# Kernel optimization log

Hardware: AMD Instinct MI355X
Metric: run time of the kernel (lower is better)

Reference implementation:

```python
import jax, jax.numpy as jnp
import numpy as np

T, B, X, Y, H, Z, D = 256, 128, 128, 256, 512, 256, 8


def setup_inputs() -> dict:
    key = jax.random.key(0)
    ks = iter(jax.random.split(key, 64))

    def p(shape, scale=0.05):
        return jax.random.normal(next(ks), shape, dtype=jnp.float32) * scale

    inp = dict(
        x=p((T, B, X), 1.0), y=p((T, B, Y), 1.0),
        W_dprior=p((D, D)), b_dprior=p((D,)),
        Wdp=p((D, D, H)), bdp=p((D, D)),
        Wq1=p((D, Z, Z + H)), bq1=p((D, Z)), Wq2=p((D, Z, Z)), bq2=p((D, Z)),
        Wqm=p((D, Z, Z)), bqm=p((D, Z)), Wqs=p((D, Z, Z)), bqs=p((D, Z)),
        Wp1=p((D, Z, Z + H)), bp1=p((D, Z)), Wp2=p((D, Z, Z)), bp2=p((D, Z)),
        Wpm=p((D, Z, Z)), bpm=p((D, Z)), Wps=p((D, Z, Z)), bps=p((D, Z)),
        We1=p((D, Y, Z + H)), be1=p((D, Y)), We2=p((D, Y, Y)), be2=p((D, Y)),
        Wem=p((D, Y, Y)), bem=p((D, Y)), Wes=p((D, Y, Y)), bes=p((D, Y)),
        Wih_f=p((3 * H, X)), Whh_f=p((3 * H, H)), bih_f=p((3 * H,)), bhh_f=p((3 * H,)),
        Wih_b=p((3 * H, Y + H)), Whh_b=p((3 * H, H)), bih_b=p((3 * H,)), bhh_b=p((3 * H,)),
    )
    return inp


def _gru(xs, Wih, Whh, bih, bhh):
    # xs: [T, B, in]; torch GRU gate order r, z, n
    h0 = jnp.zeros((xs.shape[1], Whh.shape[1]), xs.dtype)

    def cell(h, x_t):
        gi = x_t @ Wih.T + bih
        gh = h @ Whh.T + bhh
        ir, iz, inn = jnp.split(gi, 3, axis=1)
        hr, hz, hn = jnp.split(gh, 3, axis=1)
        r = jax.nn.sigmoid(ir + hr)
        zg = jax.nn.sigmoid(iz + hz)
        n = jnp.tanh(inn + r * hn)
        h_new = (1.0 - zg) * n + zg * h
        return h_new, h_new

    _, out = jax.lax.scan(cell, h0, xs)
    return out  # [T, B, H]


def _mlp2(W1, b1, W2, b2, inp):
    # inp: [B, in]; W1: [D, out, in] -> [D, B, out] with two ReLU layers
    h = jax.nn.relu(jnp.einsum('doi,bi->dbo', W1, inp) + b1[:, None, :])
    return jax.nn.relu(jnp.einsum('doi,dbi->dbo', W2, h) + b2[:, None, :])


def _head(Wm, bm, h):
    return jnp.einsum('doi,dbi->dbo', Wm, h) + bm[:, None, :]


def reference(x, y, W_dprior, b_dprior, Wdp, bdp,
              Wq1, bq1, Wq2, bq2, Wqm, bqm, Wqs, bqs,
              Wp1, bp1, Wp2, bp2, Wpm, bpm, Wps, bps,
              We1, be1, We2, be2, Wem, bem, Wes, bes,
              Wih_f, Whh_f, bih_f, bhh_f, Wih_b, Whh_b, bih_b, bhh_b):
    Tn, Bn, _ = x.shape
    Dn = W_dprior.shape[0]
    Zn = Wq1.shape[1]
    eye = jnp.eye(Dn, dtype=x.dtype)
    T0 = eye * (1.0 - 0.05 * Dn) + 0.05  # Transition_initial
    Trans = jax.nn.softmax(T0 @ W_dprior.T + b_dprior, axis=1) * 0.5 + eye * 0.5
    logT = jnp.log(Trans)

    of = _gru(x, Wih_f, Whh_f, bih_f, bhh_f)                       # [T,B,H]
    ob = _gru(jnp.flip(jnp.concatenate([y, of], 2), 0), Wih_b, Whh_b, bih_b, bhh_b)
    ob = jnp.flip(ob, 0)  # ob[t] == output_backward[T-1-t]

    d0 = jax.nn.one_hot(jax.random.categorical(jax.random.key(7), jnp.zeros((Bn, Dn))), Dn, dtype=x.dtype)
    z0 = jnp.zeros((Bn, Zn), x.dtype)
    dpost0 = jnp.full((Bn, Dn), 1.0 / Dn, x.dtype)

    def step(carry, inputs):
        d_prev, z_prev, dpost_prev, key = carry
        of_t, ob_t, y_t = inputs
        key, k1, k2 = jax.random.split(key, 3)

        # per-expert d-posterior, mixed by previous one-hot state
        dpost_all = jax.nn.softmax(jnp.einsum('dij,bj->dbi', Wdp, ob_t) + bdp[:, None, :], axis=-1)  # [D,B,D]
        d_post = jnp.einsum('dbi,bd->bi', dpost_all, d_prev)  # [B,D]
        d_new = jax.nn.one_hot(jax.random.categorical(k1, jnp.log(d_post)), Dn, dtype=x.dtype)

        # z prior (transition) experts
        hp = _mlp2(Wp1, bp1, Wp2, bp2, jnp.concatenate([of_t, z_prev], 1))
        zp_mean = _head(Wpm, bpm, hp)
        zp_std = jax.nn.softplus(_head(Wps, bps, hp))
        # z posterior experts
        hq = _mlp2(Wq1, bq1, Wq2, bq2, jnp.concatenate([ob_t, z_prev], 1))
        zq_mean = _head(Wqm, bqm, hq)
        zq_std = jax.nn.softplus(_head(Wqs, bqs, hq))

        zq_mean_mix = jnp.einsum('dbz,bd->bz', zq_mean, d_new)
        zq_std_mix = jnp.einsum('dbz,bd->bz', zq_std, d_new)
        z_t = zq_mean_mix + zq_std_mix * jax.random.normal(k2, zq_mean_mix.shape, x.dtype)

        # emission experts
        he = _mlp2(We1, be1, We2, be2, jnp.concatenate([of_t, z_t], 1))
        ye_mean = _head(Wem, bem, he)
        ye_std = jax.nn.softplus(_head(Wes, bes, he))

        # losses, weighted per expert as in the torch loop
        kldg_e = 2.0 * jnp.log(zp_std / zq_std) + (zq_std ** 2 + (zq_mean - zp_mean) ** 2) / zp_std ** 2 - 1.0
        kldg = 0.5 * jnp.einsum('dbz,bd->', kldg_e, d_post)
        kldc_e = jnp.sum(dpost_all * (jnp.log(dpost_all + 1e-8) - logT[:, None, :]), axis=-1)  # [D,B]
        kldc = jnp.einsum('db,bd->', kldc_e, dpost_prev)
        nll_e = 0.5 * (jnp.log(2.0 * jnp.pi) + 2.0 * jnp.log(ye_std) + ((y_t - ye_mean) / ye_std) ** 2)
        nll = jnp.einsum('dby,bd->', nll_e, d_post)

        return (d_new, z_t, d_post, key), (kldg, kldc, nll)

    carry0 = (d0, z0, dpost0, jax.random.key(1))
    _, (kg, kc, nl) = jax.lax.scan(step, carry0, (of, ob, y))
    return jnp.stack([jnp.sum(kg), jnp.sum(kc), jnp.sum(nl)])
```

## Files before the change

### kernel.cpp

```cpp
#include <hip/hip_runtime.h>
#include <hip/hip_bf16.h>
#include <math.h>
#include <stdint.h>

#define TT 256
#define BB 128
#define XX 128
#define YY 256
#define HH 512
#define ZZ 256
#define DD 8
#define G3 1536
#define CH 8
#define TC 32

typedef unsigned int u32;
typedef __attribute__((ext_vector_type(8))) short bf16x8;
typedef __attribute__((ext_vector_type(4))) float f32x4;

__device__ __forceinline__ uint2 tf2(uint2 key, u32 c0, u32 c1) {
  u32 ks0 = key.x, ks1 = key.y, ks2 = ks0 ^ ks1 ^ 0x1BD11BDAu;
  u32 x0 = c0 + ks0, x1 = c1 + ks1;
#define TFR(r) { x0 += x1; x1 = (x1 << r) | (x1 >> (32 - r)); x1 ^= x0; }
  TFR(13) TFR(15) TFR(26) TFR(6)  x0 += ks1; x1 += ks2 + 1u;
// ... 68 lines not shown
__device__ __forceinline__ float b2f(u32 h) { return __uint_as_float(h << 16); }

__device__ __forceinline__ short f2b(float f) {
  __hip_bfloat16 h = __float2bfloat16(f);
  return *reinterpret_cast<short*>(&h);
}

#define FMA8M(v0, v1, wv, A) do { \
  A[0]=fmaf((v0).x,(wv),A[0]); A[1]=fmaf((v0).y,(wv),A[1]); \
  A[2]=fmaf((v0).z,(wv),A[2]); A[3]=fmaf((v0).w,(wv),A[3]); \
  A[4]=fmaf((v1).x,(wv),A[4]); A[5]=fmaf((v1).y,(wv),A[5]); \
  A[6]=fmaf((v1).z,(wv),A[6]); A[7]=fmaf((v1).w,(wv),A[7]); } while(0)

#define FMA44(a4, b4, A) do { \
  A[0][0]=fmaf((a4).x,(b4).x,A[0][0]); A[0][1]=fmaf((a4).x,(b4).y,A[0][1]); A[0][2]=fmaf((a4).x,(b4).z,A[0][2]); A[0][3]=fmaf((a4).x,(b4).w,A[0][3]); \
  A[1][0]=fmaf((a4).y,(b4).x,A[1][0]); A[1][1]=fmaf((a4).y,(b4).y,A[1][1]); A[1][2]=fmaf((a4).y,(b4).z,A[1][2]); A[1][3]=fmaf((a4).y,(b4).w,A[1][3]); \
  A[2][0]=fmaf((a4).z,(b4).x,A[2][0]); A[2][1]=fmaf((a4).z,(b4).y,A[2][1]); A[2][2]=fmaf((a4).z,(b4).z,A[2][2]); A[2][3]=fmaf((a4).z,(b4).w,A[2][3]); \
  A[3][0]=fmaf((a4).w,(b4).x,A[3][0]); A[3][1]=fmaf((a4).w,(b4).y,A[3][1]); A[3][2]=fmaf((a4).w,(b4).z,A[3][2]); A[3][3]=fmaf((a4).w,(b4).w,A[3][3]); } while(0)

__global__ void k_sentinel(float* __restrict__ out) {
  if (threadIdx.x < 3) out[threadIdx.x] = 1.2345e8f;
}

__global__ void k_init1(const float* __restrict__ Wdpr, const float* __restrict__ bdpr,
                        float* __restrict__ LOGT, uint2* __restrict__ KEYS,
                        uint2* __restrict__ K1s, uint2* __restrict__ K2s) {
  int tid = threadIdx.x;
  if (tid == 0) {
    uint2 key; key.x = 0u; key.y = 1u;
    for (int t = 0; t < TT; t++) {
      KEYS[t] = key;
      uint2 e0 = tf2(key, 0u, 3u);
      uint2 e1 = tf2(key, 1u, 4u);
      key.x = e0.x; key.y = e1.x;
    }
  }
  __syncthreads();
  for (int t = tid; t < TT; t += 256) {
    uint2 key = KEYS[t];
    uint2 e0 = tf2(key, 0u, 3u);
    uint2 e1 = tf2(key, 1u, 4u);
    uint2 e2 = tf2(key, 2u, 5u);
    uint2 k1; k1.x = e2.x; k1.y = e0.y;
    uint2 k2; k2.x = e1.y; k2.y = e2.y;
    K1s[t] = k1; K2s[t] = k2;
  }
// ... 11 lines not shown
    LOGT[i * 8 + j] = logf(tr);
  }
}

__global__ void k_init2(int* __restrict__ EIDX, float* __restrict__ DP, float* __restrict__ ZT) {
  int blk = blockIdx.x, tid = threadIdx.x;
  if (blk == 0) {
    if (tid < BB) {
      uint2 k7; k7.x = 0u; k7.y = 7u;
      float best = -1e30f; int bi = 0;
      for (int i = 0; i < DD; i++) {
        float g = gumbelf(rbits(k7, tid * DD + i, BB * DD));
        if (g > best) { best = g; bi = i; }
      }
      EIDX[tid] = bi;
      for (int i = 0; i < DD; i++) DP[tid * DD + i] = 0.125f;
    }
  } else {
    int base = (blk - 1) * 1024 + tid;
    ZT[base] = 0.f; ZT[base + 256] = 0.f; ZT[base + 512] = 0.f; ZT[base + 768] = 0.f;
  }
}

template <int ACT, int OUTBF, int A0BF>
__global__ __launch_bounds__(256)
void gemm2seg(const void* __restrict__ A0v, long a0_gs, int lda0, int K0,
              const float* __restrict__ A1, long a1_gs, int lda1, int K1,
              const float* __restrict__ W, long w_gs, int ldw, int wofs,
              const float* __restrict__ bias, long b_gs,
              void* __restrict__ Cv, long c_gs, int ldc, int gdiv) {
  const int g = blockIdx.z;
  const int ga = g / gdiv, gw = g % DD;
  const float* pW = W + (long)gw * w_gs + wofs;
  const int m0 = blockIdx.x * 64, n0 = blockIdx.y * 64;
  const int tid = threadIdx.x;
  const int tm = tid >> 4, tn = tid & 15;
  __shared__ float As[32][68];
  __shared__ float Bs[32][68];
  float acc[4][4];
#pragma unroll
  for (int r = 0; r < 4; r++)
#pragma unroll
    for (int c = 0; c < 4; c++) acc[r][c] = 0.f;
  const int K = K0 + K1;
  for (int kb = 0; kb < K; kb += 32) {
#pragma unroll
    for (int l = 0; l < 2; l++) {
      int idx = tid + l * 256; int row = idx >> 3, c4 = (idx & 7) << 2;
      float4 v;
      if (kb < K0) {
        if (A0BF) {
          const __hip_bfloat16* p = (const __hip_bfloat16*)A0v + (long)ga * a0_gs + (long)(m0 + row) * lda0 + kb + c4;
          uint2 u = *(const uint2*)p;
          v.x = b2f(u.x & 0xffffu); v.y = b2f(u.x >> 16);
          v.z = b2f(u.y & 0xffffu); v.w = b2f(u.y >> 16);
        } else {
          v = *(const float4*)((const float*)A0v + (long)ga * a0_gs + (long)(m0 + row) * lda0 + kb + c4);
        }
      } else {
        v = *(const float4*)(A1 + (long)ga * a1_gs + (long)(m0 + row) * lda1 + (kb - K0) + c4);
      }
      As[c4 + 0][row] = v.x; As[c4 + 1][row] = v.y; As[c4 + 2][row] = v.z; As[c4 + 3][row] = v.w;
    }
#pragma unroll
    for (int l = 0; l < 2; l++) {
      int idx = tid + l * 256; int row = idx >> 3, c4 = (idx & 7) << 2;
      float4 v = *(const float4*)(pW + (long)(n0 + row) * ldw + kb + c4);
      Bs[c4 + 0][row] = v.x; Bs[c4 + 1][row] = v.y; Bs[c4 + 2][row] = v.z; Bs[c4 + 3][row] = v.w;
    }
    __syncthreads();
#pragma unroll
    for (int k = 0; k < 32; k++) {
      float4 a = *(const float4*)&As[k][tm << 2];
      float4 b = *(const float4*)&Bs[k][tn << 2];
      FMA44(a, b, acc);
    }
    __syncthreads();
  }
#pragma unroll
  for (int r = 0; r < 4; r++) {
    int m = m0 + (tm << 2) + r;
#pragma unroll
    for (int c = 0; c < 4; c++) {
      int n = n0 + (tn << 2) + c;
      float v = acc[r][c];
      if (bias) v += bias[(long)gw * b_gs + n];
      if (ACT == 1) v = fmaxf(v, 0.f);
      if (OUTBF) ((__hip_bfloat16*)Cv)[(long)g * c_gs + (long)m * ldc + n] = __float2bfloat16(v);
      else       ((float*)Cv)[(long)g * c_gs + (long)m * ldc + n] = v;
    }
  }
}

template <int ACT, int OUTBF, int A0BF>
__global__ __launch_bounds__(256)
void gemmMF(const void* __restrict__ A0v, long a0_gs, int lda0, int K0,
            const float* __restrict__ A1, long a1_gs, int lda1, int K1,
            const float* __restrict__ W, long w_gs, int ldw, int wofs,
            const float* __restrict__ bias, long b_gs,
            void* __restrict__ Cv, long c_gs, int ldc, int gdiv) {
  const int g = blockIdx.z;
  const int ga = g / gdiv, gw = g % DD;
  const float* pW = W + (long)gw * w_gs + wofs;
  const int m0 = blockIdx.x * 64, n0 = blockIdx.y * 64;
  const int tid = threadIdx.x;
  const int wave = tid >> 6, lane = tid & 63;
  const int wr = wave >> 1, wc = wave & 1;
  __shared__ short As[64][40];
  __shared__ short Bs[64][40];
  f32x4 acc[2][2];
#pragma unroll
  for (int a = 0; a < 2; a++)
#pragma unroll
    for (int b = 0; b < 2; b++) acc[a][b] = (f32x4)(0.f);
  const int K = K0 + K1;
  const int srow = tid >> 2;
  const int sks  = (tid & 3) << 3;
  for (int kb = 0; kb < K; kb += 32) {
    {
      bf16x8 st;
      if (kb < K0) {
        if (A0BF) {
          const short* p = (const short*)A0v + (long)ga * a0_gs + (long)(m0 + srow) * lda0 + kb + sks;
          st = *(const bf16x8*)p;
        } else {
          const float* p = (const float*)A0v + (long)ga * a0_gs + (long)(m0 + srow) * lda0 + kb + sks;
          float4 v0 = *(const float4*)p, v1 = *(const float4*)(p + 4);
          st[0]=f2b(v0.x); st[1]=f2b(v0.y); st[2]=f2b(v0.z); st[3]=f2b(v0.w);
          st[4]=f2b(v1.x); st[5]=f2b(v1.y); st[6]=f2b(v1.z); st[7]=f2b(v1.w);
        }
      } else {
        const float* p = A1 + (long)ga * a1_gs + (long)(m0 + srow) * lda1 + (kb - K0) + sks;
        float4 v0 = *(const float4*)p, v1 = *(const float4*)(p + 4);
        st[0]=f2b(v0.x); st[1]=f2b(v0.y); st[2]=f2b(v0.z); st[3]=f2b(v0.w);
        st[4]=f2b(v1.x); st[5]=f2b(v1.y); st[6]=f2b(v1.z); st[7]=f2b(v1.w);
      }
      *(bf16x8*)&As[srow][sks] = st;
    }
    {
      const float* p = pW + (long)(n0 + srow) * ldw + kb + sks;
      float4 v0 = *(const float4*)p, v1 = *(const float4*)(p + 4);
      bf16x8 st;
      st[0]=f2b(v0.x); st[1]=f2b(v0.y); st[2]=f2b(v0.z); st[3]=f2b(v0.w);
      st[4]=f2b(v1.x); st[5]=f2b(v1.y); st[6]=f2b(v1.z); st[7]=f2b(v1.w);
      *(bf16x8*)&Bs[srow][sks] = st;
    }
    __syncthreads();
    {
      const int l15 = lane & 15, kq = (lane >> 4) << 3;
      bf16x8 a0 = *(const bf16x8*)&As[wr * 32 + l15][kq];
      bf16x8 a1 = *(const bf16x8*)&As[wr * 32 + 16 + l15][kq];
      bf16x8 b0 = *(const bf16x8*)&Bs[wc * 32 + l15][kq];
      bf16x8 b1 = *(const bf16x8*)&Bs[wc * 32 + 16 + l15][kq];
      acc[0][0] = __builtin_amdgcn_mfma_f32_16x16x32_bf16(a0, b0, acc[0][0], 0, 0, 0);
      acc[0][1] = __builtin_amdgcn_mfma_f32_16x16x32_bf16(a0, b1, acc[0][1], 0, 0, 0);
      acc[1][0] = __builtin_amdgcn_mfma_f32_16x16x32_bf16(a1, b0, acc[1][0], 0, 0, 0);
      acc[1][1] = __builtin_amdgcn_mfma_f32_16x16x32_bf16(a1, b1, acc[1][1], 0, 0, 0);
    }
    __syncthreads();
  }
  const int ccol = lane & 15, crow4 = (lane >> 4) << 2;
#pragma unroll
  for (int mr = 0; mr < 2; mr++) {
#pragma unroll
    for (int nc = 0; nc < 2; nc++) {
      int n = n0 + wc * 32 + nc * 16 + ccol;
      float bv = bias ? bias[(long)gw * b_gs + n] : 0.f;
#pragma unroll
      for (int r = 0; r < 4; r++) {
        int m = m0 + wr * 32 + mr * 16 + crow4 + r;
        float v = acc[mr][nc][r] + bv;
        if (ACT == 1) v = fmaxf(v, 0.f);
        if (OUTBF) ((__hip_bfloat16*)Cv)[(long)g * c_gs + (long)m * ldc + n] = __float2bfloat16(v);
        else       ((float*)Cv)[(long)g * c_gs + (long)m * ldc + n] = v;
      }
    }
  }
}

__global__ __launch_bounds__(256)
void k_gru(const float* __restrict__ GI, const float* __restrict__ hprev,
           const float* __restrict__ Whh, const float* __restrict__ bhh,
           float* __restrict__ hout, __hip_bfloat16* __restrict__ houtB) {
  const int bt = blockIdx.x >> 5, jt = blockIdx.x & 31;
  const int b0 = bt * 16, j0 = jt * 16;
  const int tid = threadIdx.x;
  const int bi = tid >> 4, ji = tid & 15;
  __shared__ float ws[48][132];
  __shared__ float hs[16][132];
  float ar = 0.f, az = 0.f, an = 0.f;
  for (int kc = 0; kc < HH; kc += 128) {
    for (int idx = tid; idx < 48 * 32; idx += 256) {
      int r = idx >> 5, c4 = (idx & 31) << 2;
      int jr = r / 3, gr = r % 3;
      int grow = gr * HH + j0 + jr;
      *(float4*)&ws[r][c4] = *(const float4*)(Whh + (long)grow * HH + kc + c4);
    }
    for (int idx = tid; idx < 16 * 32; idx += 256) {
      int r = idx >> 5, c4 = (idx & 31) << 2;
// ... 167 lines not shown
#pragma unroll
    for (int bl = 0; bl < 8; bl++) { qm[bl] = bm_; qs[bl] = bs__; }
    for (int k = 0; k < ZZ; k += 4) {
      float4 wm4 = *(const float4*)(wm + k);
      float4 ws4 = *(const float4*)(wsd + k);
#pragma unroll
      for (int kk = 0; kk < 4; kk++) {
        float wmv = kk == 0 ? wm4.x : kk == 1 ? wm4.y : kk == 2 ? wm4.z : wm4.w;
        float wsv = kk == 0 ? ws4.x : kk == 1 ? ws4.y : kk == 2 ? ws4.z : ws4.w;
        float4 h0 = *(const float4*)&h2t[k + kk][0];
        float4 h1v = *(const float4*)&h2t[k + kk][4];
        FMA8M(h0, h1v, wmv, qm);
        FMA8M(h0, h1v, wsv, qs);
      }
    }
  }
#pragma unroll
  for (int bl = 0; bl < 8; bl++) {
    if (en_s[bl] == d) {
      int b = b0 + bl;
      float eps = normalf(rbits(K2s[t], b * ZZ + tid, BB * ZZ));
      ZT[((long)(t + 1) * BB + b) * ZZ + tid] = qm[bl] + softplusf_(qs[bl]) * eps;
    }
  }
}

__global__ __launch_bounds__(256)
void k_heads_pq(const float* __restrict__ LA, const float* __restrict__ LB,
                const float* __restrict__ Wpm, const float* __restrict__ bpm,
                const float* __restrict__ Wps, const float* __restrict__ bps,
                const float* __restrict__ Wqm, const float* __restrict__ bqm,
                const float* __restrict__ Wqs, const float* __restrict__ bqs,
                const float* __restrict__ DP, float* __restrict__ PART, int t0) {
  const int g = blockIdx.z; const int tl = g >> 3, d = g & 7; const int t = t0 + tl;
  const int m0 = blockIdx.x * 64, n0 = blockIdx.y * 64;
  const int tid = threadIdx.x; const int tm = tid >> 4, tn = tid & 15;
  __shared__ float As[32][68], W1s[32][68], W2s[32][68];
  float aPm[4][4], aPs[4][4], aQm[4][4], aQs[4][4];
#pragma unroll
  for (int r = 0; r < 4; r++)
#pragma unroll
    for (int c = 0; c < 4; c++) { aPm[r][c] = 0.f; aPs[r][c] = 0.f; aQm[r][c] = 0.f; aQs[r][c] = 0.f; }

#define HEADPASS(Abase, Wm_, Ws_, ACCM, ACCS) \
  { const float* Ap = (Abase) + (long)g * (BB * ZZ); \
    const float* Wm = (Wm_) + (long)d * ZZ * ZZ; \
    const float* Wsp = (Ws_) + (long)d * ZZ * ZZ; \
    for (int kb = 0; kb < ZZ; kb += 32) { \
      for (int l = 0; l < 2; l++) { \
        int idx = tid + l * 256; int row = idx >> 3, c4 = (idx & 7) << 2; \
        float4 v = *(const float4*)(Ap + (long)(m0 + row) * ZZ + kb + c4); \
        As[c4+0][row]=v.x; As[c4+1][row]=v.y; As[c4+2][row]=v.z; As[c4+3][row]=v.w; \
        v = *(const float4*)(Wm + (long)(n0 + row) * ZZ + kb + c4); \
        W1s[c4+0][row]=v.x; W1s[c4+1][row]=v.y; W1s[c4+2][row]=v.z; W1s[c4+3][row]=v.w; \
        v = *(const float4*)(Wsp + (long)(n0 + row) * ZZ + kb + c4); \
        W2s[c4+0][row]=v.x; W2s[c4+1][row]=v.y; W2s[c4+2][row]=v.z; W2s[c4+3][row]=v.w; \
      } \
      __syncthreads(); \
      _Pragma("unroll") \
      for (int k = 0; k < 32; k++) { \
        float4 a = *(const float4*)&As[k][tm << 2]; \
        float4 b1 = *(const float4*)&W1s[k][tn << 2]; \
        float4 b2 = *(const float4*)&W2s[k][tn << 2]; \
        FMA44(a, b1, ACCM); \
        FMA44(a, b2, ACCS); \
      } \
      __syncthreads(); \
    } }

  HEADPASS(LA, Wpm, Wps, aPm, aPs)
  HEADPASS(LB, Wqm, Wqs, aQm, aQs)

  float local = 0.f;
#pragma unroll
  for (int r = 0; r < 4; r++) {
    int b = m0 + (tm << 2) + r;
    float w8 = DP[((long)(t + 1) * BB + b) * DD + d];
#pragma unroll
    for (int c = 0; c < 4; c++) {
      int n = n0 + (tn << 2) + c;
      float pm = aPm[r][c] + bpm[d * ZZ + n];
      float ps = softplusf_(aPs[r][c] + bps[d * ZZ + n]);
      float qm = aQm[r][c] + bqm[d * ZZ + n];
      float qs = softplusf_(aQs[r][c] + bqs[d * ZZ + n]);
      float dm = qm - pm;
      local += 0.5f * w8 * (2.f * logf(ps / qs) + (qs * qs + dm * dm) / (ps * ps) - 1.f);
    }
  }
  local = wave_sum(local);
  __shared__ float red[4];
  int wid = tid >> 6;
  if ((tid & 63) == 0) red[wid] = local;
  __syncthreads();
  if (tid == 0) atomicAdd(&PART[((long)t * DD + d) * 4 + 0], red[0] + red[1] + red[2] + red[3]);
}

__global__ __launch_bounds__(256)
void k_heads_e(const float* __restrict__ LA,
               const float* __restrict__ Wem, const float* __restrict__ bem,
               const float* __restrict__ Wes, const float* __restrict__ bes,
               const float* __restrict__ yy, const float* __restrict__ DP,
               const float* __restrict__ KCE, float* __restrict__ PART, int t0) {
  const int g = blockIdx.z; const int tl = g >> 3, d = g & 7; const int t = t0 + tl;
  const int m0 = blockIdx.x * 64, n0 = blockIdx.y * 64;
  const int tid = threadIdx.x; const int tm = tid >> 4, tn = tid & 15;
  __shared__ float As[32][68], W1s[32][68], W2s[32][68];
  float aM[4][4], aS[4][4];
#pragma unroll
  for (int r = 0; r < 4; r++)
#pragma unroll
    for (int c = 0; c < 4; c++) { aM[r][c] = 0.f; aS[r][c] = 0.f; }
  {
    const float* Ap = LA + (long)g * (BB * ZZ);
    const float* Wm = Wem + (long)d * YY * YY;
    const float* Wsp = Wes + (long)d * YY * YY;
    for (int kb = 0; kb < YY; kb += 32) {
      for (int l = 0; l < 2; l++) {
        int idx = tid + l * 256; int row = idx >> 3, c4 = (idx & 7) << 2;
        float4 v = *(const float4*)(Ap + (long)(m0 + row) * YY + kb + c4);
        As[c4+0][row]=v.x; As[c4+1][row]=v.y; As[c4+2][row]=v.z; As[c4+3][row]=v.w;
        v = *(const float4*)(Wm + (long)(n0 + row) * YY + kb + c4);
        W1s[c4+0][row]=v.x; W1s[c4+1][row]=v.y; W1s[c4+2][row]=v.z; W1s[c4+3][row]=v.w;
        v = *(const float4*)(Wsp + (long)(n0 + row) * YY + kb + c4);
        W2s[c4+0][row]=v.x; W2s[c4+1][row]=v.y; W2s[c4+2][row]=v.z; W2s[c4+3][row]=v.w;
      }
      __syncthreads();
#pragma unroll
      for (int k = 0; k < 32; k++) {
        float4 a = *(const float4*)&As[k][tm << 2];
        float4 b1 = *(const float4*)&W1s[k][tn << 2];
        float4 b2 = *(const float4*)&W2s[k][tn << 2];
        FMA44(a, b1, aM);
        FMA44(a, b2, aS);
      }
      __syncthreads();
    }
  }
  float local = 0.f;
#pragma unroll
  for (int r = 0; r < 4; r++) {
    int b = m0 + (tm << 2) + r;
    float w8 = DP[((long)(t + 1) * BB + b) * DD + d];
#pragma unroll
    for (int c = 0; c < 4; c++) {
      int n = n0 + (tn << 2) + c;
      float ym = aM[r][c] + bem[d * YY + n];
      float ys = softplusf_(aS[r][c] + bes[d * YY + n]);
      float yv = yy[((long)t * BB + b) * YY + n];
      float rr = (yv - ym) / ys;
      local += w8 * 0.5f * (1.8378770664093453f + 2.f * logf(ys) + rr * rr);
    }
  }
  local = wave_sum(local);
  __shared__ float red[4];
  int wid = tid >> 6;
  if ((tid & 63) == 0) red[wid] = local;
  __syncthreads();
  if (tid == 0) atomicAdd(&PART[((long)t * DD + d) * 4 + 2], red[0] + red[1] + red[2] + red[3]);
  if (blockIdx.x == 0 && blockIdx.y == 0) {
    __syncthreads();
    float v = 0.f;
    if (tid < BB) v = KCE[((long)t * DD + d) * BB + tid] * DP[((long)t * BB + tid) * DD + d];
    v = wave_sum(v);
    if ((tid & 63) == 0) red[wid] = v;
    __syncthreads();
    if (tid == 0) atomicAdd(&PART[((long)t * DD + d) * 4 + 1], red[0] + red[1] + red[2] + red[3]);
  }
}

__global__ void k_fin(const float* __restrict__ PART, float* __restrict__ out) {
  int tid = threadIdx.x;
  float s0 = 0.f, s1 = 0.f, s2 = 0.f;
  for (int i = tid; i < TT * DD; i += 256) {
    s0 += PART[i * 4 + 0]; s1 += PART[i * 4 + 1]; s2 += PART[i * 4 + 2];
  }
  s0 = wave_sum(s0); s1 = wave_sum(s1); s2 = wave_sum(s2);
  __shared__ float r0[4], r1[4], r2[4];
  int wid = tid >> 6;
  if ((tid & 63) == 0) { r0[wid] = s0; r1[wid] = s1; r2[wid] = s2; }
  __syncthreads();
  if (tid == 0) {
    out[0] = r0[0] + r0[1] + r0[2] + r0[3];
    out[1] = r1[0] + r1[1] + r1[2] + r1[3];
    out[2] = r2[0] + r2[1] + r2[2] + r2[3];
  }
}

extern "C" void kernel_launch(void* const* d_in, const int* in_sizes, int n_in,
                              void* d_out, int out_size, void* d_ws, size_t ws_size,
// ... 39 lines not shown
  const float* bhh_b  = (const float*)d_in[37];

  char* base = (char*)d_ws;
  size_t off = 0;
  auto alloc = [&](size_t bytes) -> char* {
    char* p = base + off;
    off += (bytes + 1023) & ~(size_t)1023;
    return p;
  };
  float* LOGT = (float*)alloc(64 * 4);
  uint2* KEYS = (uint2*)alloc(TT * 8);
  uint2* K1s  = (uint2*)alloc(TT * 8);
  uint2* K2s  = (uint2*)alloc(TT * 8);
  int*   EIDX = (int*)alloc((size_t)(TT + 1) * BB * 4);
  float* DP   = (float*)alloc((size_t)(TT + 1) * BB * DD * 4);
  float* DPA  = (float*)alloc((size_t)TT * BB * DD * DD * 4);
  float* KCE  = (float*)alloc((size_t)TT * DD * BB * 4);
  float* ZT   = (float*)alloc((size_t)(TT + 1) * BB * ZZ * 4);
  float* PART = (float*)alloc((size_t)TT * DD * 4 * 4);
  float* OF   = (float*)alloc((size_t)TT * BB * HH * 4);
  __hip_bfloat16* OB = (__hip_bfloat16*)alloc((size_t)TT * BB * HH * 2);
  float* HROLL = (float*)alloc((size_t)TC * BB * HH * 4);
  char*  SH   = alloc((size_t)TC * BB * G3 * 4);
  float* GIc  = (float*)SH;
  __hip_bfloat16* OBPc = (__hip_bfloat16*)SH;
  float* LH1  = (float*)SH;
  float* LH2A = LH1 + (size_t)CH * DD * BB * ZZ;
  float* LH2B = LH2A + (size_t)CH * DD * BB * ZZ;

  if (ws_size < off) {
    k_sentinel<<<1, 64, 0, stream>>>((float*)d_out);
    return;
  }

  hipMemsetAsync(PART, 0, (size_t)TT * DD * 4 * 4, stream);
  k_init1<<<1, 256, 0, stream>>>(Wdpr, bdpr, LOGT, KEYS, K1s, K2s);
  k_init2<<<33, 256, 0, stream>>>(EIDX, DP, ZT);

  const long BH = (long)BB * HH, BZ = (long)BB * ZZ, BG = (long)BB * G3;

  for (int c = 0; c < TT / TC; c++) {
    int t0 = c * TC;
    gemm2seg<0, 0, 0><<<dim3(64, 24, 1), 256, 0, stream>>>(
        x + (long)t0 * BB * XX, 0, XX, XX, nullptr, 0, 4, 0,
        Wih_f, 0, XX, 0, bih_f, 0, GIc, 0, G3, 1);
    for (int tl = 0; tl < TC; tl++) {
      int t = t0 + tl;
      k_gru<<<256, 256, 0, stream>>>(GIc + (long)tl * BG,
                                     t ? (OF + (long)(t - 1) * BH) : nullptr,
                                     Whh_f, bhh_f, OF + (long)t * BH, nullptr);
    }
  }
  for (int c = TT / TC - 1; c >= 0; c--) {
    int t0 = c * TC;
    gemm2seg<0, 0, 0><<<dim3(64, 24, 1), 256, 0, stream>>>(
        y + (long)t0 * BB * YY, 0, YY, YY, OF + (long)t0 * BH, 0, HH, HH,
        Wih_b, 0, 768, 0, bih_b, 0, GIc, 0, G3, 1);
    for (int tl = TC - 1; tl >= 0; tl--) {
      int t = t0 + tl;
      k_gru<<<256, 256, 0, stream>>>(GIc + (long)tl * BG,
                                     (t == TT - 1) ? nullptr : (HROLL + (long)((t + 1) & (TC - 1)) * BH),
                                     Whh_b, bhh_b, HROLL + (long)(t & (TC - 1)) * BH, OB + (long)t * BH);
    }
    k_dpa<<<dim3(TC, 4), 256, 0, stream>>>(Wdp, bdp, HROLL, LOGT, DPA, KCE, t0);
  }
  k_dchain<<<1, 128, 0, stream>>>(DPA, K1s, EIDX, DP);
  for (int c = 0; c < TT / TC; c++) {
    int t0 = c * TC;
    gemmMF<0, 1, 1><<<dim3(64, 4, 8), 256, 0, stream>>>(
        OB + (long)t0 * BH, 0, HH, HH, nullptr, 0, 4, 0,
        Wq1, (long)ZZ * 768, 768, 0, nullptr, 0, OBPc, (long)TC * BB * ZZ, ZZ, 8);
    for (int tl = 0; tl < TC; tl++) {
      k_step<<<128, 256, 0, stream>>>(t0 + tl, EIDX, K2s, OBPc,
                                      Wq1, bq1, Wq2, bq2, Wqm, bqm, Wqs, bqs, ZT);
    }
  }
  for (int c = 0; c < TT / CH; c++) {
    int t0 = c * CH;
    dim3 gl(2, 4, CH * DD);
    gemmMF<1, 0, 0><<<gl, 256, 0, stream>>>(
        OF + (long)t0 * BH, BH, HH, HH, ZT + (long)t0 * BZ, BZ, ZZ, ZZ,
        Wp1, (long)ZZ * 768, 768, 0, bp1, ZZ, LH1, BZ, ZZ, 8);
    gemmMF<1, 0, 0><<<gl, 256, 0, stream>>>(
        LH1, BZ, ZZ, ZZ, nullptr, 0, 4, 0,
        Wp2, (long)ZZ * ZZ, ZZ, 0, bp2, ZZ, LH2A, BZ, ZZ, 1);
    gemmMF<1, 0, 1><<<gl, 256, 0, stream>>>(
        OB + (long)t0 * BH, BH, HH, HH, ZT + (long)t0 * BZ, BZ, ZZ, ZZ,
        Wq1, (long)ZZ * 768, 768, 0, bq1, ZZ, LH1, BZ, ZZ, 8);
    gemmMF<1, 0, 0><<<gl, 256, 0, stream>>>(
        LH1, BZ, ZZ, ZZ, nullptr, 0, 4, 0,
        Wq2, (long)ZZ * ZZ, ZZ, 0, bq2, ZZ, LH2B, BZ, ZZ, 1);
    k_heads_pq<<<gl, 256, 0, stream>>>(LH2A, LH2B, Wpm, bpm, Wps, bps,
                                       Wqm, bqm, Wqs, bqs, DP, PART, t0);
    gemmMF<1, 0, 0><<<gl, 256, 0, stream>>>(
        OF + (long)t0 * BH, BH, HH, HH, ZT + (long)(t0 + 1) * BZ, BZ, ZZ, ZZ,
        We1, (long)YY * 768, 768, 0, be1, YY, LH1, BZ, ZZ, 8);
    gemmMF<1, 0, 0><<<gl, 256, 0, stream>>>(
        LH1, BZ, ZZ, ZZ, nullptr, 0, 4, 0,
        We2, (long)YY * YY, YY, 0, be2, YY, LH2A, BZ, ZZ, 1);
    k_heads_e<<<gl, 256, 0, stream>>>(LH2A, Wem, bem, Wes, bes, y, DP, KCE, PART, t0);
  }
  k_fin<<<1, 256, 0, stream>>>(PART, (float*)d_out);
}
```

Baseline: 27.06 ms.

## Pre-convert expert weights to bf16 and move loss heads onto MFMA

Adds a conversion kernel that casts all expert MLP and head weights to bf16 once per call. The gemmMF kernels then load bf16 weights directly instead of converting on every tile. Intermediate activations are stored as bf16, and the fp32 FMA-based p/q and emission head kernels are replaced with MFMA bf16 versions. This cuts global bandwidth and conversion ALU work in the per-chunk expert loop, at the cost of lower precision in the intermediates and heads.

```diff
diff --git a/kernel.cpp b/kernel.cpp
--- a/kernel.cpp
+++ b/kernel.cpp
@@ -114,6 +114,16 @@
   if (threadIdx.x < 3) out[threadIdx.x] = 1.2345e8f;
 }
 
+__global__ void k_cvt(const float* __restrict__ s, __hip_bfloat16* __restrict__ d, int n4) {
+  int i = blockIdx.x * 256 + threadIdx.x;
+  int stride = gridDim.x * 256;
+  for (; i < n4; i += stride) {
+    const float4 v = *(const float4*)(s + (size_t)i * 4);
+    short4 o; o.x = f2b(v.x); o.y = f2b(v.y); o.z = f2b(v.z); o.w = f2b(v.w);
+    *(short4*)((short*)d + (size_t)i * 4) = o;
+  }
+}
+
 __global__ void k_init1(const float* __restrict__ Wdpr, const float* __restrict__ bdpr,
                         float* __restrict__ LOGT, uint2* __restrict__ KEYS,
                         uint2* __restrict__ K1s, uint2* __restrict__ K2s) {
@@ -171,9 +181,9 @@
   }
 }
 
-template <int ACT, int OUTBF, int A0BF>
+template <int ACT, int OUTBF>
 __global__ __launch_bounds__(256)
-void gemm2seg(const void* __restrict__ A0v, long a0_gs, int lda0, int K0,
+void gemm2seg(const float* __restrict__ A0, long a0_gs, int lda0, int K0,
               const float* __restrict__ A1, long a1_gs, int lda1, int K1,
               const float* __restrict__ W, long w_gs, int ldw, int wofs,
               const float* __restrict__ bias, long b_gs,
@@ -198,14 +208,7 @@
       int idx = tid + l * 256; int row = idx >> 3, c4 = (idx & 7) << 2;
       float4 v;
       if (kb < K0) {
-        if (A0BF) {
-          const __hip_bfloat16* p = (const __hip_bfloat16*)A0v + (long)ga * a0_gs + (long)(m0 + row) * lda0 + kb + c4;
-          uint2 u = *(const uint2*)p;
-          v.x = b2f(u.x & 0xffffu); v.y = b2f(u.x >> 16);
-          v.z = b2f(u.y & 0xffffu); v.w = b2f(u.y >> 16);
-        } else {
-          v = *(const float4*)((const float*)A0v + (long)ga * a0_gs + (long)(m0 + row) * lda0 + kb + c4);
-        }
+        v = *(const float4*)(A0 + (long)ga * a0_gs + (long)(m0 + row) * lda0 + kb + c4);
       } else {
         v = *(const float4*)(A1 + (long)ga * a1_gs + (long)(m0 + row) * lda1 + (kb - K0) + c4);
       }
@@ -245,12 +248,12 @@
 __global__ __launch_bounds__(256)
 void gemmMF(const void* __restrict__ A0v, long a0_gs, int lda0, int K0,
             const float* __restrict__ A1, long a1_gs, int lda1, int K1,
-            const float* __restrict__ W, long w_gs, int ldw, int wofs,
+            const __hip_bfloat16* __restrict__ W, long w_gs, int ldw, int wofs,
             const float* __restrict__ bias, long b_gs,
             void* __restrict__ Cv, long c_gs, int ldc, int gdiv) {
   const int g = blockIdx.z;
   const int ga = g / gdiv, gw = g % DD;
-  const float* pW = W + (long)gw * w_gs + wofs;
+  const short* pW = (const short*)W + (long)gw * w_gs + wofs;
   const int m0 = blockIdx.x * 64, n0 = blockIdx.y * 64;
   const int tid = threadIdx.x;
   const int wave = tid >> 6, lane = tid & 63;
@@ -286,14 +289,7 @@
       }
       *(bf16x8*)&As[srow][sks] = st;
     }
-    {
-      const float* p = pW + (long)(n0 + srow) * ldw + kb + sks;
-      float4 v0 = *(const float4*)p, v1 = *(const float4*)(p + 4);
-      bf16x8 st;
-      st[0]=f2b(v0.x); st[1]=f2b(v0.y); st[2]=f2b(v0.z); st[3]=f2b(v0.w);
-      st[4]=f2b(v1.x); st[5]=f2b(v1.y); st[6]=f2b(v1.z); st[7]=f2b(v1.w);
-      *(bf16x8*)&Bs[srow][sks] = st;
-    }
+    *(bf16x8*)&Bs[srow][sks] = *(const bf16x8*)(pW + (long)(n0 + srow) * ldw + kb + sks);
     __syncthreads();
     {
       const int l15 = lane & 15, kq = (lane >> 4) << 3;
@@ -324,6 +320,177 @@
         else       ((float*)Cv)[(long)g * c_gs + (long)m * ldc + n] = v;
       }
     }
+  }
+}
+
+__global__ __launch_bounds__(256)
+void k_heads_pq_mf(const __hip_bfloat16* __restrict__ LA, const __hip_bfloat16* __restrict__ LB,
+                   const __hip_bfloat16* __restrict__ Wpm, const float* __restrict__ bpm,
+                   const __hip_bfloat16* __restrict__ Wps, const float* __restrict__ bps,
+                   const __hip_bfloat16* __restrict__ Wqm, const float* __restrict__ bqm,
+                   const __hip_bfloat16* __restrict__ Wqs, const float* __restrict__ bqs,
+                   const float* __restrict__ DP, float* __restrict__ PART, int t0) {
+  const int g = blockIdx.z; const int tl = g >> 3, d = g & 7; const int t = t0 + tl;
+  const int m0 = blockIdx.x * 64, n0 = blockIdx.y * 64;
+  const int tid = threadIdx.x;
+  const int wave = tid >> 6, lane = tid & 63;
+  const int wr = wave >> 1, wc = wave & 1;
+  __shared__ short As[64][40], W1s[64][40], W2s[64][40];
+  f32x4 aPm[2][2], aPs[2][2], aQm[2][2], aQs[2][2];
+#pragma unroll
+  for (int a = 0; a < 2; a++)
+#pragma unroll
+    for (int b = 0; b < 2; b++) {
+      aPm[a][b] = (f32x4)(0.f); aPs[a][b] = (f32x4)(0.f);
+      aQm[a][b] = (f32x4)(0.f); aQs[a][b] = (f32x4)(0.f);
+    }
+  const int srow = tid >> 2, sks = (tid & 3) << 3;
+  const int l15 = lane & 15, kq = (lane >> 4) << 3;
+#pragma unroll
+  for (int pass = 0; pass < 2; pass++) {
+    const short* Ab = (const short*)(pass ? LB : LA) + (long)g * (BB * ZZ);
+    const short* W1 = (const short*)(pass ? Wqm : Wpm) + (long)d * ZZ * ZZ;
+    const short* W2 = (const short*)(pass ? Wqs : Wps) + (long)d * ZZ * ZZ;
+    for (int kb = 0; kb < ZZ; kb += 32) {
+      *(bf16x8*)&As[srow][sks]  = *(const bf16x8*)(Ab + (long)(m0 + srow) * ZZ + kb + sks);
+      *(bf16x8*)&W1s[srow][sks] = *(const bf16x8*)(W1 + (long)(n0 + srow) * ZZ + kb + sks);
+      *(bf16x8*)&W2s[srow][sks] = *(const bf16x8*)(W2 + (long)(n0 + srow) * ZZ + kb + sks);
+      __syncthreads();
+      bf16x8 a0 = *(const bf16x8*)&As[wr * 32 + l15][kq];
+      bf16x8 a1 = *(const bf16x8*)&As[wr * 32 + 16 + l15][kq];
+      bf16x8 m0f = *(const bf16x8*)&W1s[wc * 32 + l15][kq];
+      bf16x8 m1f = *(const bf16x8*)&W1s[wc * 32 + 16 + l15][kq];
+      bf16x8 s0f = *(const bf16x8*)&W2s[wc * 32 + l15][kq];
+      bf16x8 s1f = *(const bf16x8*)&W2s[wc * 32 + 16 + l15][kq];
+      if (pass == 0) {
+        aPm[0][0] = __builtin_amdgcn_mfma_f32_16x16x32_bf16(a0, m0f, aPm[0][0], 0, 0, 0);
+        aPm[0][1] = __builtin_amdgcn_mfma_f32_16x16x32_bf16(a0, m1f, aPm[0][1], 0, 0, 0);
+        aPm[1][0] = __builtin_amdgcn_mfma_f32_16x16x32_bf16(a1, m0f, aPm[1][0], 0, 0, 0);
+        aPm[1][1] = __builtin_amdgcn_mfma_f32_16x16x32_bf16(a1, m1f, aPm[1][1], 0, 0, 0);
+        aPs[0][0] = __builtin_amdgcn_mfma_f32_16x16x32_bf16(a0, s0f, aPs[0][0], 0, 0, 0);
+        aPs[0][1] = __builtin_amdgcn_mfma_f32_16x16x32_bf16(a0, s1f, aPs[0][1], 0, 0, 0);
+        aPs[1][0] = __builtin_amdgcn_mfma_f32_16x16x32_bf16(a1, s0f, aPs[1][0], 0, 0, 0);
+        aPs[1][1] = __builtin_amdgcn_mfma_f32_16x16x32_bf16(a1, s1f, aPs[1][1], 0, 0, 0);
+      } else {
+        aQm[0][0] = __builtin_amdgcn_mfma_f32_16x16x32_bf16(a0, m0f, aQm[0][0], 0, 0, 0);
+        aQm[0][1] = __builtin_amdgcn_mfma_f32_16x16x32_bf16(a0, m1f, aQm[0][1], 0, 0, 0);
+        aQm[1][0] = __builtin_amdgcn_mfma_f32_16x16x32_bf16(a1, m0f, aQm[1][0], 0, 0, 0);
+        aQm[1][1] = __builtin_amdgcn_mfma_f32_16x16x32_bf16(a1, m1f, aQm[1][1], 0, 0, 0);
+        aQs[0][0] = __builtin_amdgcn_mfma_f32_16x16x32_bf16(a0, s0f, aQs[0][0], 0, 0, 0);
+        aQs[0][1] = __builtin_amdgcn_mfma_f32_16x16x32_bf16(a0, s1f, aQs[0][1], 0, 0, 0);
+        aQs[1][0] = __builtin_amdgcn_mfma_f32_16x16x32_bf16(a1, s0f, aQs[1][0], 0, 0, 0);
+        aQs[1][1] = __builtin_amdgcn_mfma_f32_16x16x32_bf16(a1, s1f, aQs[1][1], 0, 0, 0);
+      }
+      __syncthreads();
+    }
+  }
+  const int ccol = lane & 15, crow4 = (lane >> 4) << 2;
+  float local = 0.f;
+#pragma unroll
+  for (int mr = 0; mr < 2; mr++) {
+#pragma unroll
+    for (int nc = 0; nc < 2; nc++) {
+      int n = n0 + wc * 32 + nc * 16 + ccol;
+      float bpmv = bpm[d * ZZ + n], bpsv = bps[d * ZZ + n];
+      float bqmv = bqm[d * ZZ + n], bqsv = bqs[d * ZZ + n];
+#pragma unroll
+      for (int r = 0; r < 4; r++) {
+        int m = m0 + wr * 32 + mr * 16 + crow4 + r;
+        float w8 = DP[((long)(t + 1) * BB + m) * DD + d];
+        float pm = aPm[mr][nc][r] + bpmv;
+        float ps = softplusf_(aPs[mr][nc][r] + bpsv);
+        float qm = aQm[mr][nc][r] + bqmv;
+        float qs = softplusf_(aQs[mr][nc][r] + bqsv);
+        float dm = qm - pm;
+        local += 0.5f * w8 * (2.f * logf(ps / qs) + (qs * qs + dm * dm) / (ps * ps) - 1.f);
+      }
+    }
+  }
+  local = wave_sum(local);
+  __shared__ float red[4];
+  if ((tid & 63) == 0) red[wave] = local;
+  __syncthreads();
+  if (tid == 0) atomicAdd(&PART[((long)t * DD + d) * 4 + 0], red[0] + red[1] + red[2] + red[3]);
+}
+
+__global__ __launch_bounds__(256)
+void k_heads_e_mf(const __hip_bfloat16* __restrict__ LA,
+                  const __hip_bfloat16* __restrict__ Wem, const float* __restrict__ bem,
+                  const __hip_bfloat16* __restrict__ Wes, const float* __restrict__ bes,
+                  const float* __restrict__ yy, const float* __restrict__ DP,
+                  const float* __restrict__ KCE, float* __restrict__ PART, int t0) {
+  const int g = blockIdx.z; const int tl = g >> 3, d = g & 7; const int t = t0 + tl;
+  const int m0 = blockIdx.x * 64, n0 = blockIdx.y * 64;
+  const int tid = threadIdx.x;
+  const int wave = tid >> 6, lane = tid & 63;
+  const int wr = wave >> 1, wc = wave & 1;
+  __shared__ short As[64][40], W1s[64][40], W2s[64][40];
+  f32x4 aM[2][2], aS[2][2];
+#pragma unroll
+  for (int a = 0; a < 2; a++)
+#pragma unroll
+    for (int b = 0; b < 2; b++) { aM[a][b] = (f32x4)(0.f); aS[a][b] = (f32x4)(0.f); }
+  const int srow = tid >> 2, sks = (tid & 3) << 3;
+  const int l15 = lane & 15, kq = (lane >> 4) << 3;
+  {
+    const short* Ab = (const short*)LA + (long)g * (BB * ZZ);
+    const short* W1 = (const short*)Wem + (long)d * YY * YY;
+    const short* W2 = (const short*)Wes + (long)d * YY * YY;
+    for (int kb = 0; kb < YY; kb += 32) {
+      *(bf16x8*)&As[srow][sks]  = *(const bf16x8*)(Ab + (long)(m0 + srow) * YY + kb + sks);
+      *(bf16x8*)&W1s[srow][sks] = *(const bf16x8*)(W1 + (long)(n0 + srow) * YY + kb + sks);
+      *(bf16x8*)&W2s[srow][sks] = *(const bf16x8*)(W2 + (long)(n0 + srow) * YY + kb + sks);
+      __syncthreads();
+      bf16x8 a0 = *(const bf16x8*)&As[wr * 32 + l15][kq];
+      bf16x8 a1 = *(const bf16x8*)&As[wr * 32 + 16 + l15][kq];
+      bf16x8 m0f = *(const bf16x8*)&W1s[wc * 32 + l15][kq];
+      bf16x8 m1f = *(const bf16x8*)&W1s[wc * 32 + 16 + l15][kq];
+      bf16x8 s0f = *(const bf16x8*)&W2s[wc * 32 + l15][kq];
+      bf16x8 s1f = *(const bf16x8*)&W2s[wc * 32 + 16 + l15][kq];
+      aM[0][0] = __builtin_amdgcn_mfma_f32_16x16x32_bf16(a0, m0f, aM[0][0], 0, 0, 0);
+      aM[0][1] = __builtin_amdgcn_mfma_f32_16x16x32_bf16(a0, m1f, aM[0][1], 0, 0, 0);
+      aM[1][0] = __builtin_amdgcn_mfma_f32_16x16x32_bf16(a1, m0f, aM[1][0], 0, 0, 0);
+      aM[1][1] = __builtin_amdgcn_mfma_f32_16x16x32_bf16(a1, m1f, aM[1][1], 0, 0, 0);
+      aS[0][0] = __builtin_amdgcn_mfma_f32_16x16x32_bf16(a0, s0f, aS[0][0], 0, 0, 0);
+      aS[0][1] = __builtin_amdgcn_mfma_f32_16x16x32_bf16(a0, s1f, aS[0][1], 0, 0, 0);
+      aS[1][0] = __builtin_amdgcn_mfma_f32_16x16x32_bf16(a1, s0f, aS[1][0], 0, 0, 0);
+      aS[1][1] = __builtin_amdgcn_mfma_f32_16x16x32_bf16(a1, s1f, aS[1][1], 0, 0, 0);
+      __syncthreads();
+    }
+  }
+  const int ccol = lane & 15, crow4 = (lane >> 4) << 2;
+  float local = 0.f;
+#pragma unroll
+  for (int mr = 0; mr < 2; mr++) {
+#pragma unroll
+    for (int nc = 0; nc < 2; nc++) {
+      int n = n0 + wc * 32 + nc * 16 + ccol;
+      float bmv = bem[d * YY + n], bsv = bes[d * YY + n];
+#pragma unroll
+      for (int r = 0; r < 4; r++) {
+        int m = m0 + wr * 32 + mr * 16 + crow4 + r;
+        float w8 = DP[((long)(t + 1) * BB + m) * DD + d];
+        float ym = aM[mr][nc][r] + bmv;
+        float ys = softplusf_(aS[mr][nc][r] + bsv);
+        float yv = yy[((long)t * BB + m) * YY + n];
+        float rr = (yv - ym) / ys;
+        local += w8 * 0.5f * (1.8378770664093453f + 2.f * logf(ys) + rr * rr);
+      }
+    }
+  }
+  local = wave_sum(local);
+  __shared__ float red[4];
+  if ((tid & 63) == 0) red[wave] = local;
+  __syncthreads();
+  if (tid == 0) atomicAdd(&PART[((long)t * DD + d) * 4 + 2], red[0] + red[1] + red[2] + red[3]);
+  if (blockIdx.x == 0 && blockIdx.y == 0) {
+    __syncthreads();
+    float v = 0.f;
+    if (tid < BB) v = KCE[((long)t * DD + d) * BB + tid] * DP[((long)t * BB + tid) * DD + d];
+    v = wave_sum(v);
+    if ((tid & 63) == 0) red[wave] = v;
+    __syncthreads();
+    if (tid == 0) atomicAdd(&PART[((long)t * DD + d) * 4 + 1], red[0] + red[1] + red[2] + red[3]);
   }
 }
 
@@ -537,149 +704,6 @@
       float eps = normalf(rbits(K2s[t], b * ZZ + tid, BB * ZZ));
       ZT[((long)(t + 1) * BB + b) * ZZ + tid] = qm[bl] + softplusf_(qs[bl]) * eps;
     }
-  }
-}
-
-__global__ __launch_bounds__(256)
-void k_heads_pq(const float* __restrict__ LA, const float* __restrict__ LB,
-                const float* __restrict__ Wpm, const float* __restrict__ bpm,
-                const float* __restrict__ Wps, const float* __restrict__ bps,
-                const float* __restrict__ Wqm, const float* __restrict__ bqm,
-                const float* __restrict__ Wqs, const float* __restrict__ bqs,
-                const float* __restrict__ DP, float* __restrict__ PART, int t0) {
-  const int g = blockIdx.z; const int tl = g >> 3, d = g & 7; const int t = t0 + tl;
-  const int m0 = blockIdx.x * 64, n0 = blockIdx.y * 64;
-  const int tid = threadIdx.x; const int tm = tid >> 4, tn = tid & 15;
-  __shared__ float As[32][68], W1s[32][68], W2s[32][68];
-  float aPm[4][4], aPs[4][4], aQm[4][4], aQs[4][4];
-#pragma unroll
-  for (int r = 0; r < 4; r++)
-#pragma unroll
-    for (int c = 0; c < 4; c++) { aPm[r][c] = 0.f; aPs[r][c] = 0.f; aQm[r][c] = 0.f; aQs[r][c] = 0.f; }
-
-#define HEADPASS(Abase, Wm_, Ws_, ACCM, ACCS) \
-  { const float* Ap = (Abase) + (long)g * (BB * ZZ); \
-    const float* Wm = (Wm_) + (long)d * ZZ * ZZ; \
-    const float* Wsp = (Ws_) + (long)d * ZZ * ZZ; \
-    for (int kb = 0; kb < ZZ; kb += 32) { \
-      for (int l = 0; l < 2; l++) { \
-        int idx = tid + l * 256; int row = idx >> 3, c4 = (idx & 7) << 2; \
-        float4 v = *(const float4*)(Ap + (long)(m0 + row) * ZZ + kb + c4); \
-        As[c4+0][row]=v.x; As[c4+1][row]=v.y; As[c4+2][row]=v.z; As[c4+3][row]=v.w; \
-        v = *(const float4*)(Wm + (long)(n0 + row) * ZZ + kb + c4); \
-        W1s[c4+0][row]=v.x; W1s[c4+1][row]=v.y; W1s[c4+2][row]=v.z; W1s[c4+3][row]=v.w; \
-        v = *(const float4*)(Wsp + (long)(n0 + row) * ZZ + kb + c4); \
-        W2s[c4+0][row]=v.x; W2s[c4+1][row]=v.y; W2s[c4+2][row]=v.z; W2s[c4+3][row]=v.w; \
-      } \
-      __syncthreads(); \
-      _Pragma("unroll") \
-      for (int k = 0; k < 32; k++) { \
-        float4 a = *(const float4*)&As[k][tm << 2]; \
-        float4 b1 = *(const float4*)&W1s[k][tn << 2]; \
-        float4 b2 = *(const float4*)&W2s[k][tn << 2]; \
-        FMA44(a, b1, ACCM); \
-        FMA44(a, b2, ACCS); \
-      } \
-      __syncthreads(); \
-    } }
-
-  HEADPASS(LA, Wpm, Wps, aPm, aPs)
-  HEADPASS(LB, Wqm, Wqs, aQm, aQs)
-
-  float local = 0.f;
-#pragma unroll
-  for (int r = 0; r < 4; r++) {
-    int b = m0 + (tm << 2) + r;
-    float w8 = DP[((long)(t + 1) * BB + b) * DD + d];
-#pragma unroll
-    for (int c = 0; c < 4; c++) {
-      int n = n0 + (tn << 2) + c;
-      float pm = aPm[r][c] + bpm[d * ZZ + n];
-      float ps = softplusf_(aPs[r][c] + bps[d * ZZ + n]);
-      float qm = aQm[r][c] + bqm[d * ZZ + n];
-      float qs = softplusf_(aQs[r][c] + bqs[d * ZZ + n]);
-      float dm = qm - pm;
-      local += 0.5f * w8 * (2.f * logf(ps / qs) + (qs * qs + dm * dm) / (ps * ps) - 1.f);
-    }
-  }
-  local = wave_sum(local);
-  __shared__ float red[4];
-  int wid = tid >> 6;
-  if ((tid & 63) == 0) red[wid] = local;
-  __syncthreads();
-  if (tid == 0) atomicAdd(&PART[((long)t * DD + d) * 4 + 0], red[0] + red[1] + red[2] + red[3]);
-}
-
-__global__ __launch_bounds__(256)
-void k_heads_e(const float* __restrict__ LA,
-               const float* __restrict__ Wem, const float* __restrict__ bem,
-               const float* __restrict__ Wes, const float* __restrict__ bes,
-               const float* __restrict__ yy, const float* __restrict__ DP,
-               const float* __restrict__ KCE, float* __restrict__ PART, int t0) {
-  const int g = blockIdx.z; const int tl = g >> 3, d = g & 7; const int t = t0 + tl;
-  const int m0 = blockIdx.x * 64, n0 = blockIdx.y * 64;
-  const int tid = threadIdx.x; const int tm = tid >> 4, tn = tid & 15;
-  __shared__ float As[32][68], W1s[32][68], W2s[32][68];
-  float aM[4][4], aS[4][4];
-#pragma unroll
-  for (int r = 0; r < 4; r++)
-#pragma unroll
-    for (int c = 0; c < 4; c++) { aM[r][c] = 0.f; aS[r][c] = 0.f; }
-  {
-    const float* Ap = LA + (long)g * (BB * ZZ);
-    const float* Wm = Wem + (long)d * YY * YY;
-    const float* Wsp = Wes + (long)d * YY * YY;
-    for (int kb = 0; kb < YY; kb += 32) {
-      for (int l = 0; l < 2; l++) {
-        int idx = tid + l * 256; int row = idx >> 3, c4 = (idx & 7) << 2;
-        float4 v = *(const float4*)(Ap + (long)(m0 + row) * YY + kb + c4);
-        As[c4+0][row]=v.x; As[c4+1][row]=v.y; As[c4+2][row]=v.z; As[c4+3][row]=v.w;
-        v = *(const float4*)(Wm + (long)(n0 + row) * YY + kb + c4);
-        W1s[c4+0][row]=v.x; W1s[c4+1][row]=v.y; W1s[c4+2][row]=v.z; W1s[c4+3][row]=v.w;
-        v = *(const float4*)(Wsp + (long)(n0 + row) * YY + kb + c4);
-        W2s[c4+0][row]=v.x; W2s[c4+1][row]=v.y; W2s[c4+2][row]=v.z; W2s[c4+3][row]=v.w;
-      }
-      __syncthreads();
-#pragma unroll
-      for (int k = 0; k < 32; k++) {
-        float4 a = *(const float4*)&As[k][tm << 2];
-        float4 b1 = *(const float4*)&W1s[k][tn << 2];
-        float4 b2 = *(const float4*)&W2s[k][tn << 2];
-        FMA44(a, b1, aM);
-        FMA44(a, b2, aS);
-      }
-      __syncthreads();
-    }
-  }
-  float local = 0.f;
-#pragma unroll
-  for (int r = 0; r < 4; r++) {
-    int b = m0 + (tm << 2) + r;
-    float w8 = DP[((long)(t + 1) * BB + b) * DD + d];
-#pragma unroll
-    for (int c = 0; c < 4; c++) {
-      int n = n0 + (tn << 2) + c;
-      float ym = aM[r][c] + bem[d * YY + n];
-      float ys = softplusf_(aS[r][c] + bes[d * YY + n]);
-      float yv = yy[((long)t * BB + b) * YY + n];
-      float rr = (yv - ym) / ys;
-      local += w8 * 0.5f * (1.8378770664093453f + 2.f * logf(ys) + rr * rr);
-    }
-  }
-  local = wave_sum(local);
-  __shared__ float red[4];
-  int wid = tid >> 6;
-  if ((tid & 63) == 0) red[wid] = local;
-  __syncthreads();
-  if (tid == 0) atomicAdd(&PART[((long)t * DD + d) * 4 + 2], red[0] + red[1] + red[2] + red[3]);
-  if (blockIdx.x == 0 && blockIdx.y == 0) {
-    __syncthreads();
-    float v = 0.f;
-    if (tid < BB) v = KCE[((long)t * DD + d) * BB + tid] * DP[((long)t * BB + tid) * DD + d];
-    v = wave_sum(v);
-    if ((tid & 63) == 0) red[wid] = v;
-    __syncthreads();
-    if (tid == 0) atomicAdd(&PART[((long)t * DD + d) * 4 + 1], red[0] + red[1] + red[2] + red[3]);
   }
 }
 
@@ -765,11 +789,27 @@
   __hip_bfloat16* OB = (__hip_bfloat16*)alloc((size_t)TT * BB * HH * 2);
   float* HROLL = (float*)alloc((size_t)TC * BB * HH * 4);
   char*  SH   = alloc((size_t)TC * BB * G3 * 4);
+  const size_t SL1 = (size_t)DD * ZZ * 768;
+  const size_t SL2 = (size_t)DD * ZZ * ZZ;
+  __hip_bfloat16* WB = (__hip_bfloat16*)alloc((3 * SL1 + 9 * SL2) * 2);
+  __hip_bfloat16* bWq1 = WB;
+  __hip_bfloat16* bWp1 = bWq1 + SL1;
+  __hip_bfloat16* bWe1 = bWp1 + SL1;
+  __hip_bfloat16* bWq2 = bWe1 + SL1;
+  __hip_bfloat16* bWp2 = bWq2 + SL2;
+  __hip_bfloat16* bWe2 = bWp2 + SL2;
+  __hip_bfloat16* bWqm = bWe2 + SL2;
+  __hip_bfloat16* bWqs = bWqm + SL2;
+  __hip_bfloat16* bWpm = bWqs + SL2;
+  __hip_bfloat16* bWps = bWpm + SL2;
+  __hip_bfloat16* bWem = bWps + SL2;
+  __hip_bfloat16* bWes = bWem + SL2;
+
   float* GIc  = (float*)SH;
   __hip_bfloat16* OBPc = (__hip_bfloat16*)SH;
-  float* LH1  = (float*)SH;
-  float* LH2A = LH1 + (size_t)CH * DD * BB * ZZ;
-  float* LH2B = LH2A + (size_t)CH * DD * BB * ZZ;
+  __hip_bfloat16* LH1b  = (__hip_bfloat16*)SH;
+  __hip_bfloat16* LH2Ab = LH1b + (size_t)CH * DD * BB * ZZ;
+  __hip_bfloat16* LH2Bb = LH2Ab + (size_t)CH * DD * BB * ZZ;
 
   if (ws_size < off) {
     k_sentinel<<<1, 64, 0, stream>>>((float*)d_out);
@@ -780,11 +820,22 @@
   k_init1<<<1, 256, 0, stream>>>(Wdpr, bdpr, LOGT, KEYS, K1s, K2s);
   k_init2<<<33, 256, 0, stream>>>(EIDX, DP, ZT);
 
+  auto cvt = [&](const float* s, __hip_bfloat16* dst, size_t n) {
+    int n4 = (int)(n >> 2);
+    int grid = (n4 + 255) / 256; if (grid > 1024) grid = 1024;
+    k_cvt<<<grid, 256, 0, stream>>>(s, dst, n4);
+  };
+  cvt(Wq1, bWq1, SL1); cvt(Wp1, bWp1, SL1); cvt(We1, bWe1, SL1);
+  cvt(Wq2, bWq2, SL2); cvt(Wp2, bWp2, SL2); cvt(We2, bWe2, SL2);
+  cvt(Wqm, bWqm, SL2); cvt(Wqs, bWqs, SL2);
+  cvt(Wpm, bWpm, SL2); cvt(Wps, bWps, SL2);
+  cvt(Wem, bWem, SL2); cvt(Wes, bWes, SL2);
+
   const long BH = (long)BB * HH, BZ = (long)BB * ZZ, BG = (long)BB * G3;
 
   for (int c = 0; c < TT / TC; c++) {
     int t0 = c * TC;
-    gemm2seg<0, 0, 0><<<dim3(64, 24, 1), 256, 0, stream>>>(
+    gemm2seg<0, 0><<<dim3(64, 24, 1), 256, 0, stream>>>(
         x + (long)t0 * BB * XX, 0, XX, XX, nullptr, 0, 4, 0,
         Wih_f, 0, XX, 0, bih_f, 0, GIc, 0, G3, 1);
     for (int tl = 0; tl < TC; tl++) {
@@ -796,7 +847,7 @@
   }
   for (int c = TT / TC - 1; c >= 0; c--) {
     int t0 = c * TC;
-    gemm2seg<0, 0, 0><<<dim3(64, 24, 1), 256, 0, stream>>>(
+    gemm2seg<0, 0><<<dim3(64, 24, 1), 256, 0, stream>>>(
         y + (long)t0 * BB * YY, 0, YY, YY, OF + (long)t0 * BH, 0, HH, HH,
         Wih_b, 0, 768, 0, bih_b, 0, GIc, 0, G3, 1);
     for (int tl = TC - 1; tl >= 0; tl--) {
@@ -812,7 +863,7 @@
     int t0 = c * TC;
     gemmMF<0, 1, 1><<<dim3(64, 4, 8), 256, 0, stream>>>(
         OB + (long)t0 * BH, 0, HH, HH, nullptr, 0, 4, 0,
-        Wq1, (long)ZZ * 768, 768, 0, nullptr, 0, OBPc, (long)TC * BB * ZZ, ZZ, 8);
+        bWq1, (long)ZZ * 768, 768, 0, nullptr, 0, OBPc, (long)TC * BB * ZZ, ZZ, 8);
     for (int tl = 0; tl < TC; tl++) {
       k_step<<<128, 256, 0, stream>>>(t0 + tl, EIDX, K2s, OBPc,
                                       Wq1, bq1, Wq2, bq2, Wqm, bqm, Wqs, bqs, ZT);
@@ -821,27 +872,27 @@
   for (int c = 0; c < TT / CH; c++) {
     int t0 = c * CH;
     dim3 gl(2, 4, CH * DD);
-    gemmMF<1, 0, 0><<<gl, 256, 0, stream>>>(
+    gemmMF<1, 1, 0><<<gl, 256, 0, stream>>>(
         OF + (long)t0 * BH, BH, HH, HH, ZT + (long)t0 * BZ, BZ, ZZ, ZZ,
-        Wp1, (long)ZZ * 768, 768, 0, bp1, ZZ, LH1, BZ, ZZ, 8);
-    gemmMF<1, 0, 0><<<gl, 256, 0, stream>>>(
-        LH1, BZ, ZZ, ZZ, nullptr, 0, 4, 0,
-        Wp2, (long)ZZ * ZZ, ZZ, 0, bp2, ZZ, LH2A, BZ, ZZ, 1);
-    gemmMF<1, 0, 1><<<gl, 256, 0, stream>>>(
+        bWp1, (long)ZZ * 768, 768, 0, bp1, ZZ, LH1b, BZ, ZZ, 8);
+    gemmMF<1, 1, 1><<<gl, 256, 0, stream>>>(
+        LH1b, BZ, ZZ, ZZ, nullptr, 0, 4, 0,
+        bWp2, (long)ZZ * ZZ, ZZ, 0, bp2, ZZ, LH2Ab, BZ, ZZ, 1);
+    gemmMF<1, 1, 1><<<gl, 256, 0, stream>>>(
         OB + (long)t0 * BH, BH, HH, HH, ZT + (long)t0 * BZ, BZ, ZZ, ZZ,
-        Wq1, (long)ZZ * 768, 768, 0, bq1, ZZ, LH1, BZ, ZZ, 8);
-    gemmMF<1, 0, 0><<<gl, 256, 0, stream>>>(
-        LH1, BZ, ZZ, ZZ, nullptr, 0, 4, 0,
-        Wq2, (long)ZZ * ZZ, ZZ, 0, bq2, ZZ, LH2B, BZ, ZZ, 1);
-    k_heads_pq<<<gl, 256, 0, stream>>>(LH2A, LH2B, Wpm, bpm, Wps, bps,
-                                       Wqm, bqm, Wqs, bqs, DP, PART, t0);
-    gemmMF<1, 0, 0><<<gl, 256, 0, stream>>>(
+        bWq1, (long)ZZ * 768, 768, 0, bq1, ZZ, LH1b, BZ, ZZ, 8);
+    gemmMF<1, 1, 1><<<gl, 256, 0, stream>>>(
+        LH1b, BZ, ZZ, ZZ, nullptr, 0, 4, 0,
+        bWq2, (long)ZZ * ZZ, ZZ, 0, bq2, ZZ, LH2Bb, BZ, ZZ, 1);
+    k_heads_pq_mf<<<gl, 256, 0, stream>>>(LH2Ab, LH2Bb, bWpm, bpm, bWps, bps,
+                                          bWqm, bqm, bWqs, bqs, DP, PART, t0);
+    gemmMF<1, 1, 0><<<gl, 256, 0, stream>>>(
         OF + (long)t0 * BH, BH, HH, HH, ZT + (long)(t0 + 1) * BZ, BZ, ZZ, ZZ,
-        We1, (long)YY * 768, 768, 0, be1, YY, LH1, BZ, ZZ, 8);
-    gemmMF<1, 0, 0><<<gl, 256, 0, stream>>>(
-        LH1, BZ, ZZ, ZZ, nullptr, 0, 4, 0,
-        We2, (long)YY * YY, YY, 0, be2, YY, LH2A, BZ, ZZ, 1);
-    k_heads_e<<<gl, 256, 0, stream>>>(LH2A, Wem, bem, Wes, bes, y, DP, KCE, PART, t0);
+        bWe1, (long)YY * 768, 768, 0, be1, YY, LH1b, BZ, ZZ, 8);
+    gemmMF<1, 1, 1><<<gl, 256, 0, stream>>>(
+        LH1b, BZ, ZZ, ZZ, nullptr, 0, 4, 0,
+        bWe2, (long)YY * YY, YY, 0, be2, YY, LH2Ab, BZ, ZZ, 1);
+    k_heads_e_mf<<<gl, 256, 0, stream>>>(LH2Ab, bWem, bem, bWes, bes, y, DP, KCE, PART, t0);
   }
   k_fin<<<1, 256, 0, stream>>>(PART, (float*)d_out);
 }
```

Measured after the change: 24.10 ms. 10.9% less time.
